# Kernel optimization log

Hardware: AMD Instinct MI355X
Metric: run time of the kernel (lower is better)

The kernel has to match this reference:

```python
import jax, jax.numpy as jnp
import numpy as np

B, L, H = 2, 2048, 1024
E = H * 2          # mamba_dim = model_dim * expansion_factor
K = 4              # conv kernel size
N = 16             # SSM state dim
DT_RANK = H // 8   # 128, mamba default ceil(d_model/16) scaled on d_inner


def setup_inputs() -> dict:
    key = jax.random.key(0)
    ks = jax.random.split(key, 12)
    s = lambda fan_in: 1.0 / np.sqrt(fan_in)
    return {
        "x": jax.random.normal(ks[0], (B, L, H), jnp.float32),
        "W_in": jax.random.normal(ks[1], (H, 2 * E), jnp.float32) * s(H),
        "b_in": jnp.zeros((2 * E,), jnp.float32),
        "conv_w": jax.random.normal(ks[2], (E, 1, K), jnp.float32) * s(K),  # depthwise OIH
        "conv_b": jnp.zeros((E,), jnp.float32),
        "x_proj_w": jax.random.normal(ks[3], (E, DT_RANK + 2 * N), jnp.float32) * s(E),
        "dt_proj_w": jax.random.normal(ks[4], (DT_RANK, E), jnp.float32) * s(DT_RANK),
        "dt_bias": jax.random.uniform(ks[5], (E,), jnp.float32, -4.0, -2.0),  # softplus(.) small
        "A_log": jnp.log(jnp.broadcast_to(jnp.arange(1, N + 1, dtype=jnp.float32), (E, N))),
        "D_param": jnp.ones((E,), jnp.float32),
        "W_out": jax.random.normal(ks[6], (E, H), jnp.float32) * s(E),
        "b_out": jnp.zeros((H,), jnp.float32),
    }


def _selective_scan(u, delta, A, Bm, Cm, Dp):
    # u, delta: (B,L,E); A: (E,N); Bm, Cm: (B,L,N); Dp: (E,)
    def step(h, inp):
        d_t, u_t, b_t, c_t = inp          # (B,E), (B,E), (B,N), (B,N)
        dA = jnp.exp(d_t[..., None] * A)  # (B,E,N)
        h = dA * h + (d_t * u_t)[..., None] * b_t[:, None, :]
        y = jnp.einsum("ben,bn->be", h, c_t)
        return h, y

    h0 = jnp.zeros((u.shape[0], A.shape[0], A.shape[1]), u.dtype)
    xs = (delta.transpose(1, 0, 2), u.transpose(1, 0, 2),
          Bm.transpose(1, 0, 2), Cm.transpose(1, 0, 2))
    _, ys = jax.lax.scan(step, h0, xs)    # ys: (L,B,E)
    return ys.transpose(1, 0, 2) + u * Dp


def reference(x, W_in, b_in, conv_w, conv_b, x_proj_w, dt_proj_w, dt_bias,
              A_log, D_param, W_out, b_out):
    silu = jax.nn.silu
    z = x @ W_in + b_in                    # (B,L,2E)
    xc, xr = z[..., :E], z[..., E:]
    xr = silu(xr)
    # causal depthwise conv1d: left-pad K-1 (== torch pad=K-1 then truncate to L)
    xt = xc.transpose(0, 2, 1)             # (B,E,L)
    xt = jax.lax.conv_general_dilated(
        xt, conv_w, window_strides=(1,), padding=[(K - 1, 0)],
        feature_group_count=E, dimension_numbers=("NCH", "OIH", "NCH"))
    xc = silu((xt + conv_b[None, :, None]).transpose(0, 2, 1))  # (B,L,E)
    # S6 selective SSM
    proj = xc @ x_proj_w                   # (B,L,dt_rank+2N)
    dt = proj[..., :DT_RANK]
    Bm = proj[..., DT_RANK:DT_RANK + N]
    Cm = proj[..., DT_RANK + N:]
    delta = jax.nn.softplus(dt @ dt_proj_w + dt_bias)  # (B,L,E)
    A = -jnp.exp(A_log)                    # (E,N)
    y = _selective_scan(xc, delta, A, Bm, Cm, D_param)
    y = y * xr                             # gate
    return y @ W_out + b_out
```

## Files before the change

### kernel.cpp

```cpp
#include <hip/hip_runtime.h>
#include <cstdint>

#define SL 2048
#define SE 2048
#define SB 2
#define SN 16
#define SC 64
#define ST 32

enum { EP_SPLIT_SILU = 1, EP_PARTIAL = 4 };

typedef __attribute__((ext_vector_type(8))) short bf16x8;
typedef __attribute__((ext_vector_type(4))) float f32x4;

__device__ __forceinline__ float silu_f(float x) { return x / (1.f + __expf(-x)); }
__device__ __forceinline__ float softplus_f(float x) {
    return (x > 20.f) ? x : log1pf(__expf(x));
}
__device__ __forceinline__ ushort f2bf(float f) {
    union { float f; unsigned u; } a; a.f = f;
    unsigned r = a.u + 0x7fff + ((a.u >> 16) & 1);
    return (ushort)(r >> 16);
}
__device__ __forceinline__ float bf2f(ushort u) {
    union { float f; unsigned u; } a; a.u = ((unsigned)u) << 16;
    return a.f;
}
__device__ __forceinline__ void gload16(const void* g, void* l) {
    __builtin_amdgcn_global_load_lds(
        (const __attribute__((address_space(1))) unsigned int*)g,
        (__attribute__((address_space(3))) unsigned int*)l, 16, 0, 0);
}

template <int MODE>
__device__ __forceinline__ void gemm_body(
    const ushort* __restrict__ A, const ushort* __restrict__ Bt,
    float* __restrict__ C, const float* __restrict__ bias,
    float* __restrict__ out2, int M, int N, int K, int Esplit, int KS)
{
    __shared__ ushort As[2][128 * 64];
    __shared__ ushort Bs[2][128 * 64];
    const int tid = threadIdx.x;
    const int w = tid >> 6, l = tid & 63;
    const int wr = w >> 1, wc = w & 1;
    const int m0 = blockIdx.y * 128, n0 = blockIdx.x * 128;
    const int z = blockIdx.z;
    const int kbeg = z * KS;
    const int nt = KS / 64;
    const int srow = l >> 3, scol = (l & 7) * 8;

    f32x4 acc[4][4];
#pragma unroll
    for (int m = 0; m < 4; m++)
#pragma unroll
        for (int n = 0; n < 4; n++) acc[m][n] = (f32x4)(0.f);

    auto stage = [&](int buf, int t) {
        const int k0 = kbeg + t * 64;
#pragma unroll
        for (int r = 0; r < 4; r++) {
            const int row = r * 32 + w * 8 + srow;
            int brow = n0 + row; if (brow > N - 1) brow = N - 1;
            gload16(A + (size_t)(m0 + row) * K + k0 + scol,
                    &As[buf][r * 2048 + w * 512]);
            gload16(Bt + (size_t)brow * K + k0 + scol,
                    &Bs[buf][r * 2048 + w * 512]);
        }
    };

    stage(0, 0);
    __syncthreads();

    int cur = 0;
    const int fr = l & 15, kc = (l >> 4) * 8;
    for (int t = 0; t < nt; t++) {
        if (t + 1 < nt) stage(cur ^ 1, t + 1);
#pragma unroll
        for (int kk = 0; kk < 64; kk += 32) {
            bf16x8 af[4], bfr[4];
#pragma unroll
            for (int m = 0; m < 4; m++)
                af[m] = *(const bf16x8*)&As[cur][(wr * 64 + m * 16 + fr) * 64 + kk + kc];
#pragma unroll
            for (int n = 0; n < 4; n++)
                bfr[n] = *(const bf16x8*)&Bs[cur][(wc * 64 + n * 16 + fr) * 64 + kk + kc];
#pragma unroll
            for (int m = 0; m < 4; m++)
#pragma unroll
                for (int n = 0; n < 4; n++)
                    acc[m][n] = __builtin_amdgcn_mfma_f32_16x16x32_bf16(
                        af[m], bfr[n], acc[m][n], 0, 0, 0);
        }
        __syncthreads();
        cur ^= 1;
    }

    const int cr = (l >> 4) * 4, cc = l & 15;
    float* pbase = C + (size_t)z * M * N;
#pragma unroll
    for (int m = 0; m < 4; m++) {
#pragma unroll
        for (int j = 0; j < 4; j++) {
            const int row = m0 + wr * 64 + m * 16 + cr + j;
#pragma unroll
            for (int n = 0; n < 4; n++) {
                const int col = n0 + wc * 64 + n * 16 + cc;
                float v = acc[m][n][j];
                if (MODE == EP_SPLIT_SILU) {
                    v += bias[col];
                    if (col < Esplit)
                        C[(size_t)row * Esplit + col] = v;
                    else
                        out2[(size_t)row * Esplit + (col - Esplit)] = silu_f(v);
                } else {
                    if (col < N) pbase[(size_t)row * N + col] = v;
                }
            }
        }
    }
}

__global__ __launch_bounds__(256, 2) void g1_gemm(
    const ushort* __restrict__ A, const ushort* __restrict__ Bt,
    float* __restrict__ C, const float* __restrict__ bias,
    float* __restrict__ out2, int M, int N, int K, int Esplit, int KS)
{ gemm_body<EP_SPLIT_SILU>(A, Bt, C, bias, out2, M, N, K, Esplit, KS); }

__global__ __launch_bounds__(256, 2) void g3_gemm(
    const ushort* __restrict__ A, const ushort* __restrict__ Bt,
    float* __restrict__ C, int M, int N, int K, int KS)
{ gemm_body<EP_PARTIAL>(A, Bt, C, nullptr, nullptr, M, N, K, 0, KS); }

__global__ __launch_bounds__(256, 2) void g6_gemm(
    const ushort* __restrict__ A, const ushort* __restrict__ Bt,
    float* __restrict__ C, int M, int N, int K, int KS)
{ gemm_body<EP_PARTIAL>(A, Bt, C, nullptr, nullptr, M, N, K, 0, KS); }

__global__ __launch_bounds__(256) void g4_gemm(
    const ushort* __restrict__ A, const ushort* __restrict__ Bt,
    ushort* __restrict__ draw, const float* __restrict__ bias, int M, int N)
{
    __shared__ ushort As[128 * 64];
    __shared__ ushort Bs[128 * 64];
    const int tid = threadIdx.x;
    const int w = tid >> 6, l = tid & 63;
    const int wr = w >> 1, wc = w & 1;
    const int m0 = blockIdx.y * 128, n0 = blockIdx.x * 128;
    const int srow = l >> 3, scol = (l & 7) * 8;
    const int K = 128;

    f32x4 acc[4][4];
#pragma unroll
    for (int m = 0; m < 4; m++)
#pragma unroll
        for (int n = 0; n < 4; n++) acc[m][n] = (f32x4)(0.f);

    const int fr = l & 15, kc = (l >> 4) * 8;
#pragma unroll
    for (int t = 0; t < 2; t++) {
        const int k0 = t * 64;
#pragma unroll
        for (int r = 0; r < 4; r++) {
            const int row = r * 32 + w * 8 + srow;
            gload16(A + (size_t)(m0 + row) * K + k0 + scol, &As[r * 2048 + w * 512]);
            gload16(Bt + (size_t)(n0 + row) * K + k0 + scol, &Bs[r * 2048 + w * 512]);
        }
        __syncthreads();
#pragma unroll
        for (int kk = 0; kk < 64; kk += 32) {
            bf16x8 af[4], bfr[4];
#pragma unroll
            for (int m = 0; m < 4; m++)
                af[m] = *(const bf16x8*)&As[(wr * 64 + m * 16 + fr) * 64 + kk + kc];
#pragma unroll
            for (int n = 0; n < 4; n++)
                bfr[n] = *(const bf16x8*)&Bs[(wc * 64 + n * 16 + fr) * 64 + kk + kc];
#pragma unroll
            for (int m = 0; m < 4; m++)
#pragma unroll
                for (int n = 0; n < 4; n++)
                    acc[m][n] = __builtin_amdgcn_mfma_f32_16x16x32_bf16(
                        af[m], bfr[n], acc[m][n], 0, 0, 0);
        }
        __syncthreads();
    }

    const int cr = (l >> 4) * 4, cc = l & 15;
#pragma unroll
    for (int m = 0; m < 4; m++) {
#pragma unroll
        for (int j = 0; j < 4; j++) {
            const int row = m0 + wr * 64 + m * 16 + cr + j;
#pragma unroll
            for (int n = 0; n < 4; n++) {
                const int col = n0 + wc * 64 + n * 16 + cc;
                draw[(size_t)row * N + col] = f2bf(acc[m][n][j] + bias[col]);
            }
        }
    }
}

__global__ __launch_bounds__(256) void gemm3_reduce(
    const float* __restrict__ Pp, float* __restrict__ proj,
    ushort* __restrict__ dtbf, int M, int N, int Z)
{
    const size_t g = (size_t)blockIdx.x * 256 + threadIdx.x;
    const size_t tot = (size_t)M * N;
    if (g >= tot) return;
    float s = 0.f;
    for (int z = 0; z < Z; z++) s += Pp[(size_t)z * tot + g];
    proj[g] = s;
    const int col = (int)(g % N);
    if (col < 128) {
        const size_t row = g / N;
        dtbf[row * 128 + col] = f2bf(s);
    }
}

__global__ __launch_bounds__(256) void reduce6(
    const float* __restrict__ Pp, const float* __restrict__ bias,
    float* __restrict__ out, int M, int N, int Z)
{
    const size_t g = (size_t)blockIdx.x * 256 + threadIdx.x;
    const size_t tot4 = (size_t)M * N / 4;
    if (g >= tot4) return;
    const int n4 = N / 4;
    float4 s = ((const float4*)bias)[g % n4];
    for (int z = 0; z < Z; z++) {
        float4 p = ((const float4*)Pp)[z * tot4 + g];
        s.x += p.x; s.y += p.y; s.z += p.z; s.w += p.w;
    }
    ((float4*)out)[g] = s;
}

__global__ __launch_bounds__(256) void f2bf_vec(
    const float* __restrict__ in, ushort* __restrict__ out, size_t n4)
{
    for (size_t i = (size_t)blockIdx.x * 256 + threadIdx.x; i < n4;
         i += (size_t)gridDim.x * 256) {
        float4 v = ((const float4*)in)[i];
        ushort4 o;
        o.x = f2bf(v.x); o.y = f2bf(v.y); o.z = f2bf(v.z); o.w = f2bf(v.w);
        ((ushort4*)out)[i] = o;
    }
}

__global__ __launch_bounds__(256) void f2bf_transpose(
    const float* __restrict__ W, ushort* __restrict__ Wt, int R, int Ccols)
{
    __shared__ float tile[32][33];
    const int bc = blockIdx.x * 32, br = blockIdx.y * 32;
    const int tx = threadIdx.x & 31, ty = threadIdx.x >> 5;
    for (int i = ty; i < 32; i += 8)
        tile[i][tx] = W[(size_t)(br + i) * Ccols + bc + tx];
    __syncthreads();
    for (int i = ty; i < 32; i += 8)
        Wt[(size_t)(bc + i) * R + br + tx] = f2bf(tile[tx][i]);
}

__global__ __launch_bounds__(256) void conv_silu4(
    const float* __restrict__ xin, const float* __restrict__ w,
    const float* __restrict__ cb, ushort* __restrict__ xobf,
    int Ln, int En, size_t total4)
{
    const int Eq = En >> 2;
    for (size_t idx = (size_t)blockIdx.x * 256 + threadIdx.x; idx < total4;
         idx += (size_t)gridDim.x * 256) {
        const int e4 = (int)(idx % Eq);
        const size_t row = idx / Eq;
        const int l = (int)(row % Ln);
        float4 acc = ((const float4*)cb)[e4];
        const float4 w0 = ((const float4*)w)[e4 * 4 + 0];
        const float4 w1 = ((const float4*)w)[e4 * 4 + 1];
        const float4 w2 = ((const float4*)w)[e4 * 4 + 2];
        const float4 w3 = ((const float4*)w)[e4 * 4 + 3];
        const float wt0[4] = {w0.x, w0.y, w0.z, w0.w};
        const float wt1[4] = {w1.x, w1.y, w1.z, w1.w};
        const float wt2[4] = {w2.x, w2.y, w2.z, w2.w};
        const float wt3[4] = {w3.x, w3.y, w3.z, w3.w};
#pragma unroll
        for (int k = 0; k < 4; k++) {
            if (l - 3 + k >= 0) {
                float4 xv = ((const float4*)xin)[(row - 3 + k) * Eq + e4];
                acc.x = fmaf(wt0[k], xv.x, acc.x);
                acc.y = fmaf(wt1[k], xv.y, acc.y);
                acc.z = fmaf(wt2[k], xv.z, acc.z);
                acc.w = fmaf(wt3[k], xv.w, acc.w);
            }
        }
        ushort4 o;
        o.x = f2bf(silu_f(acc.x)); o.y = f2bf(silu_f(acc.y));
        o.z = f2bf(silu_f(acc.z)); o.w = f2bf(silu_f(acc.w));
        ((ushort4*)xobf)[idx] = o;
    }
}

__global__ __launch_bounds__(256) void scan_pass1(
    const ushort* __restrict__ draw, const ushort* __restrict__ u,
    const float* __restrict__ proj, const float* __restrict__ A_log,
    float* __restrict__ Pbuf, float* __restrict__ Sbuf)
{
    __shared__ float sB[ST * SN];
    const int tid = threadIdx.x;
    const int eb = blockIdx.x & 7;
    const int c  = (blockIdx.x >> 3) & (SC - 1);
    const int b  = blockIdx.x >> 9;
    const int e  = eb * 256 + tid;
    const size_t row0 = (size_t)b * SL + c * ST;

    for (int i = tid; i < ST * SN; i += 256) {
        const int tl = i >> 4, n = i & 15;
        sB[i] = proj[(row0 + tl) * 160 + 128 + n];
    }
    __syncthreads();

    float An[SN], h[SN];
    {
        const float4* Ap = (const float4*)(A_log + (size_t)e * SN);
#pragma unroll
        for (int q = 0; q < 4; q++) {
            float4 v = Ap[q];
            An[q * 4 + 0] = -expf(v.x);
            An[q * 4 + 1] = -expf(v.y);
            An[q * 4 + 2] = -expf(v.z);
            An[q * 4 + 3] = -expf(v.w);
        }
    }
#pragma unroll
    for (int n = 0; n < SN; n++) h[n] = 0.f;

    float dsum = 0.f;
    size_t idx = row0 * SE + e;
    float d = softplus_f(bf2f(draw[idx])), uu = bf2f(u[idx]);
    for (int tl = 0; tl < ST; tl++) {
        ushort dn = 0, un = 0;
        if (tl + 1 < ST) { dn = draw[idx + SE]; un = u[idx + SE]; }
        const float du = d * uu;
        dsum += d;
#pragma unroll
        for (int n = 0; n < SN; n++) {
            const float dA = __expf(d * An[n]);
            h[n] = fmaf(dA, h[n], du * sB[tl * SN + n]);
        }
        d = softplus_f(bf2f(dn)); uu = bf2f(un); idx += SE;
    }

    const size_t ob = ((((size_t)c * SB) + b) * SE + e) * SN;
#pragma unroll
    for (int q = 0; q < 4; q++) {
        float4 pv, sv;
        pv.x = __expf(An[q * 4 + 0] * dsum); sv.x = h[q * 4 + 0];
        pv.y = __expf(An[q * 4 + 1] * dsum); sv.y = h[q * 4 + 1];
        pv.z = __expf(An[q * 4 + 2] * dsum); sv.z = h[q * 4 + 2];
        pv.w = __expf(An[q * 4 + 3] * dsum); sv.w = h[q * 4 + 3];
        *(float4*)(Pbuf + ob + q * 4) = pv;
        *(float4*)(Sbuf + ob + q * 4) = sv;
    }
}

__global__ __launch_bounds__(256) void scan_pass2(
    const float* __restrict__ Pbuf, const float* __restrict__ Sbuf,
    float* __restrict__ hinit)
{
    const size_t g = (size_t)blockIdx.x * 256 + threadIdx.x;
    const size_t stride = (size_t)SB * SE * SN;
    float h = 0.f;
    float P = Pbuf[g], S = Sbuf[g];
    for (int c = 0; c < SC; c++) {
        float Pn = 0.f, Sn = 0.f;
        if (c + 1 < SC) {
            Pn = Pbuf[(c + 1) * stride + g];
            Sn = Sbuf[(c + 1) * stride + g];
        }
        hinit[c * stride + g] = h;
        h = fmaf(P, h, S);
        P = Pn; S = Sn;
    }
}

__global__ __launch_bounds__(256) void scan_pass3(
    const ushort* __restrict__ draw, const ushort* __restrict__ u,
    const float* __restrict__ proj, const float* __restrict__ A_log,
    const float* __restrict__ Dp, const float* __restrict__ xr,
    const float* __restrict__ hinit, ushort* __restrict__ yg)
{
    __shared__ float sB[ST * SN];
    __shared__ float sC[ST * SN];
    const int tid = threadIdx.x;
    const int eb = blockIdx.x & 7;
    const int c  = (blockIdx.x >> 3) & (SC - 1);
    const int b  = blockIdx.x >> 9;
    const int e  = eb * 256 + tid;
    const size_t row0 = (size_t)b * SL + c * ST;

    for (int i = tid; i < ST * SN; i += 256) {
        const int tl = i >> 4, n = i & 15;
        sB[i] = proj[(row0 + tl) * 160 + 128 + n];
        sC[i] = proj[(row0 + tl) * 160 + 144 + n];
    }
    __syncthreads();

    float An[SN], h[SN];
    {
        const float4* Ap = (const float4*)(A_log + (size_t)e * SN);
#pragma unroll
        for (int q = 0; q < 4; q++) {
            float4 v = Ap[q];
            An[q * 4 + 0] = -expf(v.x);
            An[q * 4 + 1] = -expf(v.y);
            An[q * 4 + 2] = -expf(v.z);
            An[q * 4 + 3] = -expf(v.w);
        }
    }
    {
        const size_t ib = ((((size_t)c * SB) + b) * SE + e) * SN;
#pragma unroll
        for (int q = 0; q < 4; q++) {
            float4 v = *(const float4*)(hinit + ib + q * 4);
            h[q * 4 + 0] = v.x; h[q * 4 + 1] = v.y;
            h[q * 4 + 2] = v.z; h[q * 4 + 3] = v.w;
        }
    }
    const float De = Dp[e];

    size_t idx = row0 * SE + e;
    float d = softplus_f(bf2f(draw[idx])), uu = bf2f(u[idx]), g = xr[idx];
    for (int tl = 0; tl < ST; tl++) {
        ushort dn = 0, un = 0;
        float gn = 0.f;
        if (tl + 1 < ST) {
            dn = draw[idx + SE]; un = u[idx + SE]; gn = xr[idx + SE];
        }
        const float du = d * uu;
        float y = 0.f;
#pragma unroll
        for (int n = 0; n < SN; n++) {
            const float dA = __expf(d * An[n]);
            h[n] = fmaf(dA, h[n], du * sB[tl * SN + n]);
            y = fmaf(h[n], sC[tl * SN + n], y);
        }
        yg[idx] = f2bf((y + uu * De) * g);
        d = softplus_f(bf2f(dn)); uu = bf2f(un); g = gn; idx += SE;
    }
}

extern "C" void kernel_launch(void* const* d_in, const int* in_sizes, int n_in,
                              void* d_out, int out_size, void* d_ws, size_t ws_size,
                              hipStream_t stream)
{
    const int Bc = 2, Lc = 2048, Hc = 1024, Ec = 2048;
    const int M = Bc * Lc;
    const int PN = 160;
    const int SKZ = 8;
    const int SK6 = 2;

    const float* x        = (const float*)d_in[0];
    const float* W_in     = (const float*)d_in[1];
    const float* b_in     = (const float*)d_in[2];
    const float* conv_w   = (const float*)d_in[3];
    const float* conv_b   = (const float*)d_in[4];
    const float* x_proj_w = (const float*)d_in[5];
    const float* dt_proj_w= (const float*)d_in[6];
    const float* dt_bias  = (const float*)d_in[7];
    const float* A_log    = (const float*)d_in[8];
    const float* D_param  = (const float*)d_in[9];
    const float* W_out    = (const float*)d_in[10];
    const float* b_out    = (const float*)d_in[11];
    float* out = (float*)d_out;

    float* ws = (float*)d_ws;
    const size_t ME = (size_t)M * Ec;
    const size_t PS = (size_t)SB * SE * SC * SN;

    float* xc_raw = ws;
    float* xr     = xc_raw + ME;
    float* r2     = xr + ME;
    float* r3     = r2 + ME;
    float* proj   = r3 + ME;
    float* hinit  = proj + (size_t)M * PN;

    ushort* xbf    = (ushort*)r3;
    ushort* W_in_t = (ushort*)r2;
    ushort* xc_bf  = (ushort*)r2;
    ushort* draw   = (ushort*)r3;
    float*  Pp3    = xc_raw;
    ushort* xpw_t  = (ushort*)hinit;
    ushort* dtw_t  = (ushort*)hinit + 327680;
    ushort* dtbf   = (ushort*)hinit + 327680 + 262144;
    float*  Pbuf   = xc_raw;
    float*  Sbuf   = xc_raw + PS;
    ushort* ygbf   = (ushort*)xc_raw;
    ushort* W_out_t= (ushort*)r3;
    float*  Pp6    = xr;

    f2bf_vec<<<1024, 256, 0, stream>>>(x, xbf, (size_t)M * Hc / 4);
    f2bf_transpose<<<dim3(2 * Ec / 32, Hc / 32), 256, 0, stream>>>(
        W_in, W_in_t, Hc, 2 * Ec);
    f2bf_transpose<<<dim3(PN / 32, Ec / 32), 256, 0, stream>>>(
        x_proj_w, xpw_t, Ec, PN);
    f2bf_transpose<<<dim3(Ec / 32, 128 / 32), 256, 0, stream>>>(
        dt_proj_w, dtw_t, 128, Ec);

    g1_gemm<<<dim3(2 * Ec / 128, M / 128, 1), 256, 0, stream>>>(
        xbf, W_in_t, xc_raw, b_in, xr, M, 2 * Ec, Hc, Ec, Hc);

    conv_silu4<<<2048, 256, 0, stream>>>(
        xc_raw, conv_w, conv_b, xc_bf, Lc, Ec, ME / 4);

    g3_gemm<<<dim3(2, M / 128, SKZ), 256, 0, stream>>>(
        xc_bf, xpw_t, Pp3, M, PN, Ec, Ec / SKZ);
    gemm3_reduce<<<(M * PN + 255) / 256, 256, 0, stream>>>(
        Pp3, proj, dtbf, M, PN, SKZ);

    g4_gemm<<<dim3(Ec / 128, M / 128), 256, 0, stream>>>(
        dtbf, dtw_t, draw, dt_bias, M, Ec);

    scan_pass1<<<SB * SC * (SE / 256), 256, 0, stream>>>(
        draw, xc_bf, proj, A_log, Pbuf, Sbuf);
    scan_pass2<<<(SB * SE * SN) / 256, 256, 0, stream>>>(Pbuf, Sbuf, hinit);
    scan_pass3<<<SB * SC * (SE / 256), 256, 0, stream>>>(
        draw, xc_bf, proj, A_log, D_param, xr, hinit, ygbf);

    f2bf_transpose<<<dim3(Hc / 32, Ec / 32), 256, 0, stream>>>(
        W_out, W_out_t, Ec, Hc);

    g6_gemm<<<dim3(Hc / 128, M / 128, SK6), 256, 0, stream>>>(
        ygbf, W_out_t, Pp6, M, Hc, Ec, Ec / SK6);
    reduce6<<<(int)((size_t)M * Hc / 4 + 255) / 256, 256, 0, stream>>>(
        Pp6, b_out, out, M, Hc, SK6);
}
```

Measured before the change: 312.0 us.

## Single-buffer GEMM LDS, drop occupancy hint, fuse bias into unsplit output GEMM

The shared GEMM body moves from double-buffered LDS staging with prefetch of the next K tile to a single buffer with load, sync, compute, sync. This halves LDS use, which may allow more resident blocks. The launch-bounds occupancy hint of 2 is removed from the three GEMM kernels. The final output GEMM no longer uses split-K with a separate reduction kernel; it runs with one K slice and adds the bias in its epilogue. That removes the partial-buffer round trip, but it gives up overlap of global loads with MFMA work and cuts the final GEMM's grid in half.

Result: no change. 316.7 us (+1.5%).

```diff
diff --git a/kernel.cpp b/kernel.cpp
--- a/kernel.cpp
+++ b/kernel.cpp
@@ -8,7 +8,7 @@
 #define SC 64
 #define ST 32
 
-enum { EP_SPLIT_SILU = 1, EP_PARTIAL = 4 };
+enum { EP_SPLIT_SILU = 1, EP_BIAS = 3, EP_PARTIAL = 4 };
 
 typedef __attribute__((ext_vector_type(8))) short bf16x8;
 typedef __attribute__((ext_vector_type(4))) float f32x4;
@@ -38,8 +38,8 @@
     float* __restrict__ C, const float* __restrict__ bias,
     float* __restrict__ out2, int M, int N, int K, int Esplit, int KS)
 {
-    __shared__ ushort As[2][128 * 64];
-    __shared__ ushort Bs[2][128 * 64];
+    __shared__ ushort As[128 * 64];
+    __shared__ ushort Bs[128 * 64];
     const int tid = threadIdx.x;
     const int w = tid >> 6, l = tid & 63;
     const int wr = w >> 1, wc = w & 1;
@@ -48,6 +48,7 @@
     const int kbeg = z * KS;
     const int nt = KS / 64;
     const int srow = l >> 3, scol = (l & 7) * 8;
+    const int fr = l & 15, kc = (l >> 4) * 8;
 
     f32x4 acc[4][4];
 #pragma unroll
@@ -55,35 +56,27 @@
 #pragma unroll
         for (int n = 0; n < 4; n++) acc[m][n] = (f32x4)(0.f);
 
-    auto stage = [&](int buf, int t) {
+    for (int t = 0; t < nt; t++) {
         const int k0 = kbeg + t * 64;
 #pragma unroll
         for (int r = 0; r < 4; r++) {
             const int row = r * 32 + w * 8 + srow;
             int brow = n0 + row; if (brow > N - 1) brow = N - 1;
             gload16(A + (size_t)(m0 + row) * K + k0 + scol,
-                    &As[buf][r * 2048 + w * 512]);
+                    &As[r * 2048 + w * 512]);
             gload16(Bt + (size_t)brow * K + k0 + scol,
-                    &Bs[buf][r * 2048 + w * 512]);
-        }
-    };
-
-    stage(0, 0);
-    __syncthreads();
-
-    int cur = 0;
-    const int fr = l & 15, kc = (l >> 4) * 8;
-    for (int t = 0; t < nt; t++) {
-        if (t + 1 < nt) stage(cur ^ 1, t + 1);
+                    &Bs[r * 2048 + w * 512]);
+        }
+        __syncthreads();
 #pragma unroll
         for (int kk = 0; kk < 64; kk += 32) {
             bf16x8 af[4], bfr[4];
 #pragma unroll
             for (int m = 0; m < 4; m++)
-                af[m] = *(const bf16x8*)&As[cur][(wr * 64 + m * 16 + fr) * 64 + kk + kc];
+                af[m] = *(const bf16x8*)&As[(wr * 64 + m * 16 + fr) * 64 + kk + kc];
 #pragma unroll
             for (int n = 0; n < 4; n++)
-                bfr[n] = *(const bf16x8*)&Bs[cur][(wc * 64 + n * 16 + fr) * 64 + kk + kc];
+                bfr[n] = *(const bf16x8*)&Bs[(wc * 64 + n * 16 + fr) * 64 + kk + kc];
 #pragma unroll
             for (int m = 0; m < 4; m++)
 #pragma unroll
@@ -92,7 +85,6 @@
                         af[m], bfr[n], acc[m][n], 0, 0, 0);
         }
         __syncthreads();
-        cur ^= 1;
     }
 
     const int cr = (l >> 4) * 4, cc = l & 15;
@@ -112,6 +104,8 @@
                         C[(size_t)row * Esplit + col] = v;
                     else
                         out2[(size_t)row * Esplit + (col - Esplit)] = silu_f(v);
+                } else if (MODE == EP_BIAS) {
+                    C[(size_t)row * N + col] = v + bias[col];
                 } else {
                     if (col < N) pbase[(size_t)row * N + col] = v;
                 }
@@ -120,21 +114,22 @@
     }
 }
 
-__global__ __launch_bounds__(256, 2) void g1_gemm(
+__global__ __launch_bounds__(256) void g1_gemm(
     const ushort* __restrict__ A, const ushort* __restrict__ Bt,
     float* __restrict__ C, const float* __restrict__ bias,
     float* __restrict__ out2, int M, int N, int K, int Esplit, int KS)
 { gemm_body<EP_SPLIT_SILU>(A, Bt, C, bias, out2, M, N, K, Esplit, KS); }
 
-__global__ __launch_bounds__(256, 2) void g3_gemm(
+__global__ __launch_bounds__(256) void g3_gemm(
     const ushort* __restrict__ A, const ushort* __restrict__ Bt,
     float* __restrict__ C, int M, int N, int K, int KS)
 { gemm_body<EP_PARTIAL>(A, Bt, C, nullptr, nullptr, M, N, K, 0, KS); }
 
-__global__ __launch_bounds__(256, 2) void g6_gemm(
+__global__ __launch_bounds__(256) void g6_gemm(
     const ushort* __restrict__ A, const ushort* __restrict__ Bt,
-    float* __restrict__ C, int M, int N, int K, int KS)
-{ gemm_body<EP_PARTIAL>(A, Bt, C, nullptr, nullptr, M, N, K, 0, KS); }
+    float* __restrict__ C, const float* __restrict__ bias,
+    int M, int N, int K, int KS)
+{ gemm_body<EP_BIAS>(A, Bt, C, bias, nullptr, M, N, K, 0, KS); }
 
 __global__ __launch_bounds__(256) void g4_gemm(
     const ushort* __restrict__ A, const ushort* __restrict__ Bt,
@@ -215,22 +210,6 @@
         const size_t row = g / N;
         dtbf[row * 128 + col] = f2bf(s);
     }
-}
-
-__global__ __launch_bounds__(256) void reduce6(
-    const float* __restrict__ Pp, const float* __restrict__ bias,
-    float* __restrict__ out, int M, int N, int Z)
-{
-    const size_t g = (size_t)blockIdx.x * 256 + threadIdx.x;
-    const size_t tot4 = (size_t)M * N / 4;
-    if (g >= tot4) return;
-    const int n4 = N / 4;
-    float4 s = ((const float4*)bias)[g % n4];
-    for (int z = 0; z < Z; z++) {
-        float4 p = ((const float4*)Pp)[z * tot4 + g];
-        s.x += p.x; s.y += p.y; s.z += p.z; s.w += p.w;
-    }
-    ((float4*)out)[g] = s;
 }
 
 __global__ __launch_bounds__(256) void f2bf_vec(
@@ -452,7 +431,6 @@
     const int M = Bc * Lc;
     const int PN = 160;
     const int SKZ = 8;
-    const int SK6 = 2;
 
     const float* x        = (const float*)d_in[0];
     const float* W_in     = (const float*)d_in[1];
@@ -491,7 +469,6 @@
     float*  Sbuf   = xc_raw + PS;
     ushort* ygbf   = (ushort*)xc_raw;
     ushort* W_out_t= (ushort*)r3;
-    float*  Pp6    = xr;
 
     f2bf_vec<<<1024, 256, 0, stream>>>(x, xbf, (size_t)M * Hc / 4);
     f2bf_transpose<<<dim3(2 * Ec / 32, Hc / 32), 256, 0, stream>>>(
@@ -524,8 +501,6 @@
     f2bf_transpose<<<dim3(Hc / 32, Ec / 32), 256, 0, stream>>>(
         W_out, W_out_t, Ec, Hc);
 
-    g6_gemm<<<dim3(Hc / 128, M / 128, SK6), 256, 0, stream>>>(
-        ygbf, W_out_t, Pp6, M, Hc, Ec, Ec / SK6);
-    reduce6<<<(int)((size_t)M * Hc / 4 + 255) / 256, 256, 0, stream>>>(
-        Pp6, b_out, out, M, Hc, SK6);
-}
+    g6_gemm<<<dim3(Hc / 128, M / 128, 1), 256, 0, stream>>>(
+        ygbf, W_out_t, out, b_out, M, Hc, Ec, Ec);
+}
```

## Add 256x256-tile 512-thread GEMM for input and output projections

Applied to the files above, without the earlier changes.

Adds a new templated GEMM kernel with 256x256 block tiles, 8 waves, BK=32 and explicit vmcnt waits plus raw barriers for double buffering. It replaces the 128x128 kernels for the input projection (with the split/SiLU epilogue) and the output projection, whose split-K factor rises from 2 to 4. The intent is more data reuse per LDS load and fewer blocks. The small x_proj GEMM now uses a single-buffered 128x128 path. Risks: heavier register pressure at one block per CU, a 4-way partial buffer reusing the xr workspace that may exceed its size, and some unused leftover kernel stubs.

Result: no change. 310.8 us (-0.4%).

```diff
diff --git a/kernel.cpp b/kernel.cpp
--- a/kernel.cpp
+++ b/kernel.cpp
@@ -8,7 +8,7 @@
 #define SC 64
 #define ST 32
 
-enum { EP_SPLIT_SILU = 1, EP_PARTIAL = 4 };
+enum { EP_SPLIT_SILU = 1, EP_BIAS = 3, EP_PARTIAL = 4 };
 
 typedef __attribute__((ext_vector_type(8))) short bf16x8;
 typedef __attribute__((ext_vector_type(4))) float f32x4;
@@ -33,75 +33,80 @@
 }
 
 template <int MODE>
-__device__ __forceinline__ void gemm_body(
+__global__ __launch_bounds__(512, 1) void hgemm256c(
     const ushort* __restrict__ A, const ushort* __restrict__ Bt,
     float* __restrict__ C, const float* __restrict__ bias,
     float* __restrict__ out2, int M, int N, int K, int Esplit, int KS)
 {
-    __shared__ ushort As[2][128 * 64];
-    __shared__ ushort Bs[2][128 * 64];
+    __shared__ ushort As[2][256 * 32];
+    __shared__ ushort Bs[2][256 * 32];
     const int tid = threadIdx.x;
     const int w = tid >> 6, l = tid & 63;
-    const int wr = w >> 1, wc = w & 1;
-    const int m0 = blockIdx.y * 128, n0 = blockIdx.x * 128;
+    const int wr = w >> 2, wc = w & 3;
+    const int m0 = blockIdx.y * 256, n0 = blockIdx.x * 256;
     const int z = blockIdx.z;
     const int kbeg = z * KS;
-    const int nt = KS / 64;
-    const int srow = l >> 3, scol = (l & 7) * 8;
-
-    f32x4 acc[4][4];
-#pragma unroll
-    for (int m = 0; m < 4; m++)
+    const int nt = KS / 32;
+    const int srow = l >> 2;
+    const int scol = (l & 3) * 8;
+
+    f32x4 acc[8][4];
+#pragma unroll
+    for (int m = 0; m < 8; m++)
 #pragma unroll
         for (int n = 0; n < 4; n++) acc[m][n] = (f32x4)(0.f);
 
     auto stage = [&](int buf, int t) {
-        const int k0 = kbeg + t * 64;
-#pragma unroll
-        for (int r = 0; r < 4; r++) {
-            const int row = r * 32 + w * 8 + srow;
+        const int k0 = kbeg + t * 32;
+#pragma unroll
+        for (int r = 0; r < 2; r++) {
+            const int row = w * 32 + r * 16 + srow;
             int brow = n0 + row; if (brow > N - 1) brow = N - 1;
             gload16(A + (size_t)(m0 + row) * K + k0 + scol,
-                    &As[buf][r * 2048 + w * 512]);
+                    &As[buf][(w * 32 + r * 16) * 32]);
             gload16(Bt + (size_t)brow * K + k0 + scol,
-                    &Bs[buf][r * 2048 + w * 512]);
+                    &Bs[buf][(w * 32 + r * 16) * 32]);
         }
     };
 
     stage(0, 0);
-    __syncthreads();
 
     int cur = 0;
     const int fr = l & 15, kc = (l >> 4) * 8;
     for (int t = 0; t < nt; t++) {
-        if (t + 1 < nt) stage(cur ^ 1, t + 1);
-#pragma unroll
-        for (int kk = 0; kk < 64; kk += 32) {
-            bf16x8 af[4], bfr[4];
-#pragma unroll
-            for (int m = 0; m < 4; m++)
-                af[m] = *(const bf16x8*)&As[cur][(wr * 64 + m * 16 + fr) * 64 + kk + kc];
+        if (t + 1 < nt) {
+            stage(cur ^ 1, t + 1);
+            asm volatile("s_waitcnt vmcnt(4)" ::: "memory");
+        } else {
+            asm volatile("s_waitcnt vmcnt(0)" ::: "memory");
+        }
+        __builtin_amdgcn_s_barrier();
+
+        bf16x8 af[8], bfr[4];
+#pragma unroll
+        for (int m = 0; m < 8; m++)
+            af[m] = *(const bf16x8*)&As[cur][(wr * 128 + m * 16 + fr) * 32 + kc];
+#pragma unroll
+        for (int n = 0; n < 4; n++)
+            bfr[n] = *(const bf16x8*)&Bs[cur][(wc * 64 + n * 16 + fr) * 32 + kc];
+#pragma unroll
+        for (int m = 0; m < 8; m++)
 #pragma unroll
             for (int n = 0; n < 4; n++)
-                bfr[n] = *(const bf16x8*)&Bs[cur][(wc * 64 + n * 16 + fr) * 64 + kk + kc];
-#pragma unroll
-            for (int m = 0; m < 4; m++)
-#pragma unroll
-                for (int n = 0; n < 4; n++)
-                    acc[m][n] = __builtin_amdgcn_mfma_f32_16x16x32_bf16(
-                        af[m], bfr[n], acc[m][n], 0, 0, 0);
-        }
-        __syncthreads();
+                acc[m][n] = __builtin_amdgcn_mfma_f32_16x16x32_bf16(
+                    af[m], bfr[n], acc[m][n], 0, 0, 0);
+
+        __builtin_amdgcn_s_barrier();
         cur ^= 1;
     }
 
     const int cr = (l >> 4) * 4, cc = l & 15;
     float* pbase = C + (size_t)z * M * N;
 #pragma unroll
-    for (int m = 0; m < 4; m++) {
+    for (int m = 0; m < 8; m++) {
 #pragma unroll
         for (int j = 0; j < 4; j++) {
-            const int row = m0 + wr * 64 + m * 16 + cr + j;
+            const int row = m0 + wr * 128 + m * 16 + cr + j;
 #pragma unroll
             for (int n = 0; n < 4; n++) {
                 const int col = n0 + wc * 64 + n * 16 + cc;
@@ -120,18 +125,95 @@
     }
 }
 
-__global__ __launch_bounds__(256, 2) void g1_gemm(
+__global__ __launch_bounds__(512, 1) void g1_gemm(
+    const ushort* __restrict__ A, const ushort* __restrict__ Bt,
+    float* __restrict__ C, const float* __restrict__ bias,
+    float* __restrict__ out2, int M, int N, int K, int Esplit, int KS);
+
+template <int MODE>
+__device__ __forceinline__ void gemm_body(
     const ushort* __restrict__ A, const ushort* __restrict__ Bt,
     float* __restrict__ C, const float* __restrict__ bias,
     float* __restrict__ out2, int M, int N, int K, int Esplit, int KS)
-{ gemm_body<EP_SPLIT_SILU>(A, Bt, C, bias, out2, M, N, K, Esplit, KS); }
-
-__global__ __launch_bounds__(256, 2) void g3_gemm(
+{
+    __shared__ ushort As[128 * 64];
+    __shared__ ushort Bs[128 * 64];
+    const int tid = threadIdx.x;
+    const int w = tid >> 6, l = tid & 63;
+    const int wr = w >> 1, wc = w & 1;
+    const int m0 = blockIdx.y * 128, n0 = blockIdx.x * 128;
+    const int z = blockIdx.z;
+    const int kbeg = z * KS;
+    const int nt = KS / 64;
+    const int srow = l >> 3, scol = (l & 7) * 8;
+    const int fr = l & 15, kc = (l >> 4) * 8;
+
+    f32x4 acc[4][4];
+#pragma unroll
+    for (int m = 0; m < 4; m++)
+#pragma unroll
+        for (int n = 0; n < 4; n++) acc[m][n] = (f32x4)(0.f);
+
+    for (int t = 0; t < nt; t++) {
+        const int k0 = kbeg + t * 64;
+#pragma unroll
+        for (int r = 0; r < 4; r++) {
+            const int row = r * 32 + w * 8 + srow;
+            int brow = n0 + row; if (brow > N - 1) brow = N - 1;
+            gload16(A + (size_t)(m0 + row) * K + k0 + scol,
+                    &As[r * 2048 + w * 512]);
+            gload16(Bt + (size_t)brow * K + k0 + scol,
+                    &Bs[r * 2048 + w * 512]);
+        }
+        __syncthreads();
+#pragma unroll
+        for (int kk = 0; kk < 64; kk += 32) {
+            bf16x8 af[4], bfr[4];
+#pragma unroll
+            for (int m = 0; m < 4; m++)
+                af[m] = *(const bf16x8*)&As[(wr * 64 + m * 16 + fr) * 64 + kk + kc];
+#pragma unroll
+            for (int n = 0; n < 4; n++)
+                bfr[n] = *(const bf16x8*)&Bs[(wc * 64 + n * 16 + fr) * 64 + kk + kc];
+#pragma unroll
+            for (int m = 0; m < 4; m++)
+#pragma unroll
+                for (int n = 0; n < 4; n++)
+                    acc[m][n] = __builtin_amdgcn_mfma_f32_16x16x32_bf16(
+                        af[m], bfr[n], acc[m][n], 0, 0, 0);
+        }
+        __syncthreads();
+    }
+
+    const int cr = (l >> 4) * 4, cc = l & 15;
+    float* pbase = C + (size_t)z * M * N;
+#pragma unroll
+    for (int m = 0; m < 4; m++) {
+#pragma unroll
+        for (int j = 0; j < 4; j++) {
+            const int row = m0 + wr * 64 + m * 16 + cr + j;
+#pragma unroll
+            for (int n = 0; n < 4; n++) {
+                const int col = n0 + wc * 64 + n * 16 + cc;
+                float v = acc[m][n][j];
+                if (MODE == EP_BIAS) {
+                    C[(size_t)row * N + col] = v + bias[col];
+                } else {
+                    if (col < N) pbase[(size_t)row * N + col] = v;
+                }
+            }
+        }
+    }
+}
+
+__global__ __launch_bounds__(512, 1) void g1_gemm256(
     const ushort* __restrict__ A, const ushort* __restrict__ Bt,
-    float* __restrict__ C, int M, int N, int K, int KS)
-{ gemm_body<EP_PARTIAL>(A, Bt, C, nullptr, nullptr, M, N, K, 0, KS); }
-
-__global__ __launch_bounds__(256, 2) void g6_gemm(
+    float* __restrict__ C, const float* __restrict__ bias,
+    float* __restrict__ out2, int M, int N, int K, int Esplit, int KS)
+{
+}
+
+__global__ __launch_bounds__(256) void g3_gemm(
     const ushort* __restrict__ A, const ushort* __restrict__ Bt,
     float* __restrict__ C, int M, int N, int K, int KS)
 { gemm_body<EP_PARTIAL>(A, Bt, C, nullptr, nullptr, M, N, K, 0, KS); }
@@ -452,7 +534,7 @@
     const int M = Bc * Lc;
     const int PN = 160;
     const int SKZ = 8;
-    const int SK6 = 2;
+    const int SK6 = 4;
 
     const float* x        = (const float*)d_in[0];
     const float* W_in     = (const float*)d_in[1];
@@ -501,7 +583,7 @@
     f2bf_transpose<<<dim3(Ec / 32, 128 / 32), 256, 0, stream>>>(
         dt_proj_w, dtw_t, 128, Ec);
 
-    g1_gemm<<<dim3(2 * Ec / 128, M / 128, 1), 256, 0, stream>>>(
+    hgemm256c<EP_SPLIT_SILU><<<dim3(2 * Ec / 256, M / 256, 1), 512, 0, stream>>>(
         xbf, W_in_t, xc_raw, b_in, xr, M, 2 * Ec, Hc, Ec, Hc);
 
     conv_silu4<<<2048, 256, 0, stream>>>(
@@ -524,8 +606,8 @@
     f2bf_transpose<<<dim3(Hc / 32, Ec / 32), 256, 0, stream>>>(
         W_out, W_out_t, Ec, Hc);
 
-    g6_gemm<<<dim3(Hc / 128, M / 128, SK6), 256, 0, stream>>>(
-        ygbf, W_out_t, Pp6, M, Hc, Ec, Ec / SK6);
+    hgemm256c<EP_PARTIAL><<<dim3(Hc / 256, M / 256, SK6), 512, 0, stream>>>(
+        ygbf, W_out_t, Pp6, nullptr, nullptr, M, Hc, Ec, 0, Ec / SK6);
     reduce6<<<(int)((size_t)M * Hc / 4 + 255) / 256, 256, 0, stream>>>(
         Pp6, b_out, out, M, Hc, SK6);
 }
```
